# Performance work log

Hardware: AMD Instinct MI355X
Metric: run time of the kernel (lower is better)

## Reference

```python
import jax, jax.numpy as jnp
import numpy as np

SIG_LEVEL = 2
N_UNITS = 1024
INPUT_SIZE = 512
SIGSIZE = sum(2 ** k for k in range(1, SIG_LEVEL + 1))  # siglength(2, L) = 2^(L+1)-2 = 6
SAVED_LEN = N_UNITS * (1 + SIGSIZE)  # 7168
BATCH = 4096


def sigjoin(prev_sigs, disp, time_lapse, level):
    """Chen's identity: new_sig = prev_sig (tensor-mult) exp(v), truncated at `level`.

    prev_sigs: [N, SIGSIZE] flat signature levels (level k occupies 2^k entries),
    disp: [N, 1] displacement in dim 0; dim 1 displacement fixed to time_lapse.
    """
    N = prev_sigs.shape[0]
    v = jnp.concatenate([disp, jnp.full_like(disp, 1.0) * time_lapse], axis=1)  # [N, 2]
    # signature of the straight segment: seg_k = v^{(x)k} / k!
    seg = [v]
    for k in range(2, level + 1):
        seg.append((seg[-1][:, :, None] * v[:, None, :]).reshape(N, -1) / k)
    # split prev signature into levels
    S, off = [], 0
    for k in range(1, level + 1):
        sz = 2 ** k
        S.append(prev_sigs[:, off:off + sz])
        off += sz
    # result_k = S_k + seg_k + sum_{i=1}^{k-1} S_i (x) seg_{k-i}
    out = []
    for k in range(1, level + 1):
        r = S[k - 1] + seg[k - 1]
        for i in range(1, k):
            r = r + (S[i - 1][:, :, None] * seg[k - i - 1][:, None, :]).reshape(N, 2 ** k)
        out.append(r)
    return jnp.concatenate(out, axis=1)


def setup_inputs() -> dict:
    key = jax.random.key(0)
    ks = jax.random.split(key, 8)
    x = jax.random.normal(ks[0], (BATCH, INPUT_SIZE), dtype=jnp.float32)
    prev_sigs = jax.random.normal(ks[1], (BATCH, N_UNITS * SIGSIZE), dtype=jnp.float32) * 0.1
    prev_states = jax.random.normal(ks[2], (BATCH, N_UNITS), dtype=jnp.float32)
    W_w = jax.random.normal(ks[3], (N_UNITS, INPUT_SIZE), dtype=jnp.float32) / np.sqrt(INPUT_SIZE)
    W_b = jax.random.normal(ks[4], (N_UNITS,), dtype=jnp.float32) * 0.01
    U_w = jax.random.normal(ks[5], (N_UNITS, SAVED_LEN), dtype=jnp.float32) / np.sqrt(SAVED_LEN)
    U_b = jax.random.normal(ks[6], (N_UNITS,), dtype=jnp.float32) * 0.01
    log_timelapse = jnp.array([np.log(0.1)], dtype=jnp.float32)
    return {"x": x, "prev_sigs": prev_sigs, "prev_states": prev_states,
            "W_w": W_w, "W_b": W_b, "U_w": U_w, "U_b": U_b,
            "log_timelapse": log_timelapse}


def reference(x, prev_sigs, prev_states, W_w, W_b, U_w, U_b, log_timelapse):
    h = x @ W_w.T + W_b                                  # [B, n_units]
    mem = jnp.concatenate([prev_sigs, prev_states], 1)   # [B, saved_len]
    raw = h + mem @ U_w.T + U_b                          # [B, n_units]
    disp = (raw - prev_states).reshape(-1, 1)            # [B*n_units, 1]
    tl = jnp.exp(log_timelapse)[0]
    sigs = sigjoin(prev_sigs.reshape(-1, SIGSIZE), disp, tl, SIG_LEVEL)
    sigs = sigs.reshape(-1, N_UNITS * SIGSIZE)
    # output_signatures=True: output = [sigs, raw_output]
    return jnp.concatenate([sigs, raw], axis=1)          # [B, n_units*(sigsize+1)]
```

## Files before the change

### kernel.cpp

```cpp
#include <hip/hip_runtime.h>
#include <hip/hip_bf16.h>
#include <cmath>

#define BATCH   4096
#define NUNITS  1024
#define INSIZE  512
#define SIGSZ   6
#define KSIG    (NUNITS * SIGSZ)
#define SAVED   (KSIG + NUNITS)
#define KTOT    (INSIZE + KSIG + NUNITS)
#define OUTW    (NUNITS * (SIGSZ + 1))
#define NKT     (KTOT / 64)

#define WS_AX 0LL
#define WS_AS 2097152LL
#define WS_AT 27262976LL
#define WS_BW 31457280LL
#define WS_BU 31981568LL
#define WS_ELEMS 39321600LL
#define WS_BYTES (WS_ELEMS * 2)

typedef __attribute__((ext_vector_type(8))) short bf16x8;
typedef __attribute__((ext_vector_type(8))) unsigned short u16x8;
typedef __attribute__((ext_vector_type(4))) float f32x4;

__device__ __forceinline__ unsigned short f2bf(float f) {
    union { float f; unsigned int u; } c; c.f = f;
    unsigned int u = c.u;
    return (unsigned short)((u + 0x7FFFu + ((u >> 16) & 1u)) >> 16);
}
__device__ __forceinline__ float bf2f(unsigned short h) {
    union { unsigned int u; float f; } c; c.u = ((unsigned int)h) << 16;
    return c.f;
}

__device__ __forceinline__ int swz(int row, int bytecol) {
    return row * 64 + (((bytecol) ^ ((row & 7) << 4)) >> 1);
}

__global__ __launch_bounds__(256)
void prepack(const float* __restrict__ x, const float* __restrict__ sigs,
             const float* __restrict__ states, const float* __restrict__ Ww,
             const float* __restrict__ Uw, unsigned short* __restrict__ ws)
{
    const long long stride = (long long)gridDim.x * blockDim.x;
    for (long long p = (long long)blockIdx.x * blockDim.x + threadIdx.x;
         p < 4915200LL; p += stride) {
        const float* src; unsigned short* dst; long long o;
        if (p < 262144LL)       { src = x;      dst = ws + WS_AX; o = p; }
        else if (p < 3407872LL) { src = sigs;   dst = ws + WS_AS; o = p - 262144LL; }
        else if (p < 3932160LL) { src = states; dst = ws + WS_AT; o = p - 3407872LL; }
        else if (p < 3997696LL) { src = Ww;     dst = ws + WS_BW; o = p - 3932160LL; }
        else                    { src = Uw;     dst = ws + WS_BU; o = p - 3997696LL; }
        const float4 v0 = *(const float4*)(src + o * 8);
        const float4 v1 = *(const float4*)(src + o * 8 + 4);
        u16x8 h;
        h[0] = f2bf(v0.x); h[1] = f2bf(v0.y); h[2] = f2bf(v0.z); h[3] = f2bf(v0.w);
        h[4] = f2bf(v1.x); h[5] = f2bf(v1.y); h[6] = f2bf(v1.z); h[7] = f2bf(v1.w);
        *(u16x8*)(dst + o * 8) = h;
    }
}

#define GLD_LDS(G, L) __builtin_amdgcn_global_load_lds(                        \
        (const __attribute__((address_space(1))) unsigned int*)(G),           \
        (__attribute__((address_space(3))) unsigned int*)(L), 16, 0, 0)

__global__ __launch_bounds__(1024, 1)
void rsig_gemm(const unsigned short* __restrict__ ws,
               const float* __restrict__ states,
               const float* __restrict__ Wb,
               const float* __restrict__ Ub,
               const float* __restrict__ lt,
               float* __restrict__ out)
{
    __shared__ unsigned short lds[3 * 16384];

    const int t  = threadIdx.x;
    const int bn = blockIdx.x & 7;
    const int bm = blockIdx.x >> 3;

    const int lane = t & 63;
    const int w    = t >> 6;
    const int wm   = w >> 3;
    const int wn   = (w >> 1) & 3;
    const int wk   = w & 1;
    const int lr   = lane & 15;
    const int lg   = lane >> 4;

    const unsigned short* wsAx = ws + WS_AX;
    const unsigned short* wsAs = ws + WS_AS;
    const unsigned short* wsAt = ws + WS_AT;
    const unsigned short* wsBw = ws + WS_BW;
    const unsigned short* wsBu = ws + WS_BU;

    const int sRow = lane >> 3;
    const int sCol = 8 * ((lane & 7) ^ sRow);

    f32x4 acc[4][2];
#pragma unroll
    for (int m = 0; m < 4; ++m)
#pragma unroll
        for (int n = 0; n < 2; ++n)
            acc[m][n] = (f32x4)0.f;

#define STAGE(BUF, KT)                                                                  \
    {                                                                                   \
        const int kt_ = (KT);                                                           \
        const unsigned short* abase; int astr, koff;                                    \
        if (kt_ < 8)        { abase = wsAx; astr = INSIZE; koff = kt_ * 64; }           \
        else if (kt_ < 104) { abase = wsAs; astr = KSIG;   koff = kt_ * 64 - 512; }     \
        else                { abase = wsAt; astr = NUNITS; koff = kt_ * 64 - 6656; }    \
        const unsigned short* bbase; int bstr, koffb;                                   \
        if (kt_ < 8)        { bbase = wsBw; bstr = INSIZE; koffb = kt_ * 64; }          \
        else                { bbase = wsBu; bstr = SAVED;  koffb = kt_ * 64 - 512; }    \
        unsigned short* base = &lds[(BUF) * 16384];                                     \
        const unsigned short* ga = abase                                                \
            + (size_t)(bm * 128 + w * 8 + sRow) * astr + koff + sCol;                   \
        GLD_LDS(ga, base + w * 512);                                                    \
        const unsigned short* gb = bbase                                                \
            + (size_t)(bn * 128 + w * 8 + sRow) * bstr + koffb + sCol;                  \
        GLD_LDS(gb, base + 8192 + w * 512);                                             \
    }

    STAGE(0, 0);
    STAGE(1, 1);

    int cur = 0;
    for (int kt = 0; kt < NKT; ++kt) {
        if (kt < NKT - 1) { asm volatile("s_waitcnt vmcnt(2)" ::: "memory"); }
        else              { asm volatile("s_waitcnt vmcnt(0)" ::: "memory"); }
        __builtin_amdgcn_s_barrier();
        __builtin_amdgcn_sched_barrier(0);

        if (kt + 2 < NKT) {
            int nb = cur + 2; if (nb >= 3) nb -= 3;
            STAGE(nb, kt + 2);
        }

        {
            const unsigned short* aT = &lds[cur * 16384];
            const unsigned short* bT = aT + 8192;
            bf16x8 af[4], bfr[2];
#pragma unroll
            for (int m = 0; m < 4; ++m)
                af[m] = *(const bf16x8*)&aT[swz(wm * 64 + m * 16 + lr, wk * 64 + lg * 16)];
#pragma unroll
            for (int n = 0; n < 2; ++n)
                bfr[n] = *(const bf16x8*)&bT[swz(wn * 32 + n * 16 + lr, wk * 64 + lg * 16)];
#pragma unroll
            for (int m = 0; m < 4; ++m)
#pragma unroll
                for (int n = 0; n < 2; ++n)
                    acc[m][n] = __builtin_amdgcn_mfma_f32_16x16x32_bf16(af[m], bfr[n], acc[m][n], 0, 0, 0);
        }

        cur = (cur == 2) ? 0 : cur + 1;
    }

    __syncthreads();

    float* rawt = (float*)lds;
    if (wk == 0) {
#pragma unroll
        for (int n = 0; n < 2; ++n) {
            const int cc = wn * 32 + n * 16 + lr;
            const int ug = bn * 128 + cc;
            const float bias = Wb[ug] + Ub[ug];
#pragma unroll
            for (int m = 0; m < 4; ++m) {
                const int rr = wm * 64 + m * 16 + lg * 4;
#pragma unroll
                for (int i = 0; i < 4; ++i)
                    rawt[(rr + i) * 132 + cc] = acc[m][n][i] + bias;
            }
        }
    }
    __syncthreads();
    if (wk == 1) {
#pragma unroll
        for (int n = 0; n < 2; ++n) {
            const int cc = wn * 32 + n * 16 + lr;
#pragma unroll
            for (int m = 0; m < 4; ++m) {
                const int rr = wm * 64 + m * 16 + lg * 4;
#pragma unroll
                for (int i = 0; i < 4; ++i)
                    rawt[(rr + i) * 132 + cc] += acc[m][n][i];
            }
        }
    }
    __syncthreads();

    const float tl = expf(lt[0]);
    const int r0 = t >> 8;
    const int c  = t & 255;

    for (int pass = 0; pass < 32; ++pass) {
        const int r = pass * 4 + r0;
        const long long b = (long long)bm * 128 + r;
        if (c < 192) {
            const int u  = (2 * c) / 3;
            const int cs = c % 3;
            const unsigned short* srow = wsAs + b * KSIG + bn * 768;
            const float* strow = states + b * NUNITS + bn * 128;
            const ushort4 sin = *(const ushort4*)(srow + c * 4);
            const float e0 = bf2f(sin.x), e1 = bf2f(sin.y);
            const float e2 = bf2f(sin.z), e3 = bf2f(sin.w);
            float4 o;
            if (cs == 0) {
                const float d = rawt[r * 132 + u] - strow[u];
                o.x = e0 + d;
                o.y = e1 + tl;
                o.z = e2 + d  * (0.5f * d  + e0);
                o.w = e3 + tl * (0.5f * d  + e0);
            } else if (cs == 1) {
                const float d  = rawt[r * 132 + u]     - strow[u];
                const float dn = rawt[r * 132 + u + 1] - strow[u + 1];
                const float s1 = bf2f(srow[u * 6 + 1]);
                o.x = e0 + d  * (0.5f * tl + s1);
                o.y = e1 + tl * (0.5f * tl + s1);
                o.z = e2 + dn;
                o.w = e3 + tl;
            } else {
                const float d = rawt[r * 132 + u] - strow[u];
                const unsigned int sv = *(const unsigned int*)(srow + u * 6);
                const float s0 = bf2f((unsigned short)(sv & 0xffffu));
                const float s1 = bf2f((unsigned short)(sv >> 16));
                o.x = e0 + d  * (0.5f * d  + s0);
                o.y = e1 + tl * (0.5f * d  + s0);
                o.z = e2 + d  * (0.5f * tl + s1);
                o.w = e3 + tl * (0.5f * tl + s1);
            }
            *(float4*)(out + b * OUTW + bn * 768 + c * 4) = o;
        } else if (c < 224) {
            const int cc = (c - 192) * 4;
            const float4 rv = *(const float4*)&rawt[r * 132 + cc];
            *(float4*)(out + b * OUTW + KSIG + bn * 128 + cc) = rv;
        }
    }
#undef STAGE
}

extern "C" void kernel_launch(void* const* d_in, const int* in_sizes, int n_in,
                              void* d_out, int out_size, void* d_ws, size_t ws_size,
                              hipStream_t stream) {
    const float* x      = (const float*)d_in[0];
    const float* sigs   = (const float*)d_in[1];
    const float* states = (const float*)d_in[2];
    const float* Ww     = (const float*)d_in[3];
    const float* Wb     = (const float*)d_in[4];
    const float* Uw     = (const float*)d_in[5];
    const float* Ub     = (const float*)d_in[6];
    const float* lt     = (const float*)d_in[7];
    float* out = (float*)d_out;

    unsigned short* ws = (unsigned short*)d_ws;
    hipLaunchKernelGGL(prepack, dim3(2048), dim3(256), 0, stream,
                       x, sigs, states, Ww, Uw, ws);
    hipLaunchKernelGGL(rsig_gemm, dim3(256), dim3(1024), 0, stream,
                       ws, states, Wb, Ub, lt, out);
}
```

Before: 149.8 us.

## Use BK=128 double-buffered tiles with 4-way K split and nontemporal loads/stores

Doubles the K-tile to 128, so there are half as many loop iterations and barriers, and moves from a 3-stage to a 2-stage LDS ring. Waves are regrouped into 2×2×4 (m, n, k-split) with 4×4 MFMA accumulators per wave. Fragments are read into registers before a barrier, and only then is the next stage issued into the same buffer. The prepack loads and the epilogue stores use nontemporal hints to reduce cache pollution, and the k-split reduction now runs over 4 serialized slots. The extra barrier per iteration reduces overlap, and the larger accumulator set raises register pressure.

```diff
diff --git a/kernel.cpp b/kernel.cpp
--- a/kernel.cpp
+++ b/kernel.cpp
@@ -10,7 +10,7 @@
 #define SAVED   (KSIG + NUNITS)
 #define KTOT    (INSIZE + KSIG + NUNITS)
 #define OUTW    (NUNITS * (SIGSZ + 1))
-#define NKT     (KTOT / 64)
+#define NKT     (KTOT / 128)
 
 #define WS_AX 0LL
 #define WS_AS 2097152LL
@@ -52,11 +52,11 @@
         else if (p < 3932160LL) { src = states; dst = ws + WS_AT; o = p - 3407872LL; }
         else if (p < 3997696LL) { src = Ww;     dst = ws + WS_BW; o = p - 3932160LL; }
         else                    { src = Uw;     dst = ws + WS_BU; o = p - 3997696LL; }
-        const float4 v0 = *(const float4*)(src + o * 8);
-        const float4 v1 = *(const float4*)(src + o * 8 + 4);
+        const f32x4 v0 = __builtin_nontemporal_load((const f32x4*)(src + o * 8));
+        const f32x4 v1 = __builtin_nontemporal_load((const f32x4*)(src + o * 8) + 1);
         u16x8 h;
-        h[0] = f2bf(v0.x); h[1] = f2bf(v0.y); h[2] = f2bf(v0.z); h[3] = f2bf(v0.w);
-        h[4] = f2bf(v1.x); h[5] = f2bf(v1.y); h[6] = f2bf(v1.z); h[7] = f2bf(v1.w);
+        h[0] = f2bf(v0[0]); h[1] = f2bf(v0[1]); h[2] = f2bf(v0[2]); h[3] = f2bf(v0[3]);
+        h[4] = f2bf(v1[0]); h[5] = f2bf(v1[1]); h[6] = f2bf(v1[2]); h[7] = f2bf(v1[3]);
         *(u16x8*)(dst + o * 8) = h;
     }
 }
@@ -73,7 +73,7 @@
                const float* __restrict__ lt,
                float* __restrict__ out)
 {
-    __shared__ unsigned short lds[3 * 16384];
+    __shared__ unsigned short lds[2 * 32768];
 
     const int t  = threadIdx.x;
     const int bn = blockIdx.x & 7;
@@ -82,8 +82,8 @@
     const int lane = t & 63;
     const int w    = t >> 6;
     const int wm   = w >> 3;
-    const int wn   = (w >> 1) & 3;
-    const int wk   = w & 1;
+    const int wn   = (w >> 2) & 1;
+    const int wk   = w & 3;
     const int lr   = lane & 15;
     const int lg   = lane >> 4;
 
@@ -95,101 +95,99 @@
 
     const int sRow = lane >> 3;
     const int sCol = 8 * ((lane & 7) ^ sRow);
-
-    f32x4 acc[4][2];
+    const int rowg = w * 8 + sRow;
+    const int loAx = rowg * INSIZE + sCol;
+    const int loAs = rowg * KSIG   + sCol;
+    const int loAt = rowg * NUNITS + sCol;
+    const int loBw = rowg * INSIZE + sCol;
+    const int loBu = rowg * SAVED  + sCol;
+
+    f32x4 acc[4][4];
 #pragma unroll
     for (int m = 0; m < 4; ++m)
 #pragma unroll
-        for (int n = 0; n < 2; ++n)
+        for (int n = 0; n < 4; ++n)
             acc[m][n] = (f32x4)0.f;
 
-#define STAGE(BUF, KT)                                                                  \
-    {                                                                                   \
-        const int kt_ = (KT);                                                           \
-        const unsigned short* abase; int astr, koff;                                    \
-        if (kt_ < 8)        { abase = wsAx; astr = INSIZE; koff = kt_ * 64; }           \
-        else if (kt_ < 104) { abase = wsAs; astr = KSIG;   koff = kt_ * 64 - 512; }     \
-        else                { abase = wsAt; astr = NUNITS; koff = kt_ * 64 - 6656; }    \
-        const unsigned short* bbase; int bstr, koffb;                                   \
-        if (kt_ < 8)        { bbase = wsBw; bstr = INSIZE; koffb = kt_ * 64; }          \
-        else                { bbase = wsBu; bstr = SAVED;  koffb = kt_ * 64 - 512; }    \
-        unsigned short* base = &lds[(BUF) * 16384];                                     \
-        const unsigned short* ga = abase                                                \
-            + (size_t)(bm * 128 + w * 8 + sRow) * astr + koff + sCol;                   \
-        GLD_LDS(ga, base + w * 512);                                                    \
-        const unsigned short* gb = bbase                                                \
-            + (size_t)(bn * 128 + w * 8 + sRow) * bstr + koffb + sCol;                  \
-        GLD_LDS(gb, base + 8192 + w * 512);                                             \
+#define STAGE(BUF, KT)                                                                   \
+    {                                                                                    \
+        const int kt_ = (KT);                                                            \
+        const unsigned short* abase; long long asg; int la;                              \
+        if (kt_ < 4)       { abase = wsAx; asg = (long long)bm*128*INSIZE + kt_*128;       la = loAx; } \
+        else if (kt_ < 52) { abase = wsAs; asg = (long long)bm*128*KSIG  + kt_*128 - 512;  la = loAs; } \
+        else               { abase = wsAt; asg = (long long)bm*128*NUNITS+ kt_*128 - 6656; la = loAt; } \
+        const unsigned short* bbase; long long bsg; int lb;                              \
+        if (kt_ < 4)       { bbase = wsBw; bsg = (long long)bn*128*INSIZE + kt_*128;       lb = loBw; } \
+        else               { bbase = wsBu; bsg = (long long)bn*128*SAVED + kt_*128 - 512;  lb = loBu; } \
+        unsigned short* base = &lds[(BUF) * 32768];                                      \
+        GLD_LDS(abase + asg + la,      base +         w * 512);                          \
+        GLD_LDS(abase + asg + la + 64, base +  8192 + w * 512);                          \
+        GLD_LDS(bbase + bsg + lb,      base + 16384 + w * 512);                          \
+        GLD_LDS(bbase + bsg + lb + 64, base + 24576 + w * 512);                          \
     }
 
     STAGE(0, 0);
     STAGE(1, 1);
 
-    int cur = 0;
     for (int kt = 0; kt < NKT; ++kt) {
-        if (kt < NKT - 1) { asm volatile("s_waitcnt vmcnt(2)" ::: "memory"); }
+        if (kt < NKT - 1) { asm volatile("s_waitcnt vmcnt(4)" ::: "memory"); }
         else              { asm volatile("s_waitcnt vmcnt(0)" ::: "memory"); }
         __builtin_amdgcn_s_barrier();
         __builtin_amdgcn_sched_barrier(0);
 
-        if (kt + 2 < NKT) {
-            int nb = cur + 2; if (nb >= 3) nb -= 3;
-            STAGE(nb, kt + 2);
-        }
-
-        {
-            const unsigned short* aT = &lds[cur * 16384];
-            const unsigned short* bT = aT + 8192;
-            bf16x8 af[4], bfr[2];
-#pragma unroll
-            for (int m = 0; m < 4; ++m)
-                af[m] = *(const bf16x8*)&aT[swz(wm * 64 + m * 16 + lr, wk * 64 + lg * 16)];
-#pragma unroll
-            for (int n = 0; n < 2; ++n)
-                bfr[n] = *(const bf16x8*)&bT[swz(wn * 32 + n * 16 + lr, wk * 64 + lg * 16)];
-#pragma unroll
-            for (int m = 0; m < 4; ++m)
-#pragma unroll
-                for (int n = 0; n < 2; ++n)
-                    acc[m][n] = __builtin_amdgcn_mfma_f32_16x16x32_bf16(af[m], bfr[n], acc[m][n], 0, 0, 0);
-        }
-
-        cur = (cur == 2) ? 0 : cur + 1;
+        const int cur = kt & 1;
+        const unsigned short* aT = &lds[cur * 32768 + (wk >> 1) * 8192];
+        const unsigned short* bT = aT + 16384;
+        const int bc = (wk & 1) * 64 + lg * 16;
+
+        bf16x8 af[4], bfr[4];
+#pragma unroll
+        for (int m = 0; m < 4; ++m)
+            af[m] = *(const bf16x8*)&aT[swz(wm * 64 + m * 16 + lr, bc)];
+#pragma unroll
+        for (int n = 0; n < 4; ++n)
+            bfr[n] = *(const bf16x8*)&bT[swz(wn * 64 + n * 16 + lr, bc)];
+
+        asm volatile("s_waitcnt lgkmcnt(0)" ::: "memory");
+        __builtin_amdgcn_sched_barrier(0);
+        __builtin_amdgcn_s_barrier();
+
+        if (kt + 2 < NKT) STAGE(cur, kt + 2);
+
+#pragma unroll
+        for (int m = 0; m < 4; ++m)
+#pragma unroll
+            for (int n = 0; n < 4; ++n)
+                acc[m][n] = __builtin_amdgcn_mfma_f32_16x16x32_bf16(af[m], bfr[n], acc[m][n], 0, 0, 0);
     }
 
     __syncthreads();
 
     float* rawt = (float*)lds;
-    if (wk == 0) {
-#pragma unroll
-        for (int n = 0; n < 2; ++n) {
-            const int cc = wn * 32 + n * 16 + lr;
-            const int ug = bn * 128 + cc;
-            const float bias = Wb[ug] + Ub[ug];
-#pragma unroll
-            for (int m = 0; m < 4; ++m) {
-                const int rr = wm * 64 + m * 16 + lg * 4;
-#pragma unroll
-                for (int i = 0; i < 4; ++i)
-                    rawt[(rr + i) * 132 + cc] = acc[m][n][i] + bias;
+#pragma unroll
+    for (int slot = 0; slot < 4; ++slot) {
+        if (wk == slot) {
+#pragma unroll
+            for (int n = 0; n < 4; ++n) {
+                const int cc = wn * 64 + n * 16 + lr;
+#pragma unroll
+                for (int m = 0; m < 4; ++m) {
+                    const int rr = wm * 64 + m * 16 + lg * 4;
+                    if (slot == 0) {
+                        const float bias = Wb[bn * 128 + cc] + Ub[bn * 128 + cc];
+#pragma unroll
+                        for (int i = 0; i < 4; ++i)
+                            rawt[(rr + i) * 132 + cc] = acc[m][n][i] + bias;
+                    } else {
+#pragma unroll
+                        for (int i = 0; i < 4; ++i)
+                            rawt[(rr + i) * 132 + cc] += acc[m][n][i];
+                    }
+                }
             }
         }
-    }
-    __syncthreads();
-    if (wk == 1) {
-#pragma unroll
-        for (int n = 0; n < 2; ++n) {
-            const int cc = wn * 32 + n * 16 + lr;
-#pragma unroll
-            for (int m = 0; m < 4; ++m) {
-                const int rr = wm * 64 + m * 16 + lg * 4;
-#pragma unroll
-                for (int i = 0; i < 4; ++i)
-                    rawt[(rr + i) * 132 + cc] += acc[m][n][i];
-            }
-        }
-    }
-    __syncthreads();
+        __syncthreads();
+    }
 
     const float tl = expf(lt[0]);
     const int r0 = t >> 8;
@@ -206,36 +204,36 @@
             const ushort4 sin = *(const ushort4*)(srow + c * 4);
             const float e0 = bf2f(sin.x), e1 = bf2f(sin.y);
             const float e2 = bf2f(sin.z), e3 = bf2f(sin.w);
-            float4 o;
+            f32x4 o;
             if (cs == 0) {
                 const float d = rawt[r * 132 + u] - strow[u];
-                o.x = e0 + d;
-                o.y = e1 + tl;
-                o.z = e2 + d  * (0.5f * d  + e0);
-                o.w = e3 + tl * (0.5f * d  + e0);
+                o[0] = e0 + d;
+                o[1] = e1 + tl;
+                o[2] = e2 + d  * (0.5f * d  + e0);
+                o[3] = e3 + tl * (0.5f * d  + e0);
             } else if (cs == 1) {
                 const float d  = rawt[r * 132 + u]     - strow[u];
                 const float dn = rawt[r * 132 + u + 1] - strow[u + 1];
                 const float s1 = bf2f(srow[u * 6 + 1]);
-                o.x = e0 + d  * (0.5f * tl + s1);
-                o.y = e1 + tl * (0.5f * tl + s1);
-                o.z = e2 + dn;
-                o.w = e3 + tl;
+                o[0] = e0 + d  * (0.5f * tl + s1);
+                o[1] = e1 + tl * (0.5f * tl + s1);
+                o[2] = e2 + dn;
+                o[3] = e3 + tl;
             } else {
                 const float d = rawt[r * 132 + u] - strow[u];
                 const unsigned int sv = *(const unsigned int*)(srow + u * 6);
                 const float s0 = bf2f((unsigned short)(sv & 0xffffu));
                 const float s1 = bf2f((unsigned short)(sv >> 16));
-                o.x = e0 + d  * (0.5f * d  + s0);
-                o.y = e1 + tl * (0.5f * d  + s0);
-                o.z = e2 + d  * (0.5f * tl + s1);
-                o.w = e3 + tl * (0.5f * tl + s1);
+                o[0] = e0 + d  * (0.5f * d  + s0);
+                o[1] = e1 + tl * (0.5f * d  + s0);
+                o[2] = e2 + d  * (0.5f * tl + s1);
+                o[3] = e3 + tl * (0.5f * tl + s1);
             }
-            *(float4*)(out + b * OUTW + bn * 768 + c * 4) = o;
+            __builtin_nontemporal_store(o, (f32x4*)(out + b * OUTW + bn * 768 + c * 4));
         } else if (c < 224) {
             const int cc = (c - 192) * 4;
-            const float4 rv = *(const float4*)&rawt[r * 132 + cc];
-            *(float4*)(out + b * OUTW + KSIG + bn * 128 + cc) = rv;
+            const f32x4 rv = *(const f32x4*)&rawt[r * 132 + cc];
+            __builtin_nontemporal_store(rv, (f32x4*)(out + b * OUTW + KSIG + bn * 128 + cc));
         }
     }
 #undef STAGE
```

Result: slower. 186.2 us (+24.3%).

## Switch GEMM to 32x32x16 MFMA with K-tile 128, 4-way split-K, double buffer

Applied to the files above, without the earlier changes.

The main GEMM loop now uses 32x32x16 bf16 MFMA instructions on a 128-wide K tile instead of 16x16x32 on a 64-wide tile. Waves are regrouped into 2 N-groups by 4 K-slices, with a new XOR swizzle for the LDS layout. The three-stage pipeline becomes a double buffer with a full vmcnt(0) wait each iteration, and the split-K reduction through LDS grows from 2 to 4 serialized passes. The prepack kernel switches to nontemporal loads. The aim is to halve loop iterations and barriers and get better MFMA efficiency, at the cost of less prefetch depth and extra reduction passes.

```diff
diff --git a/kernel.cpp b/kernel.cpp
--- a/kernel.cpp
+++ b/kernel.cpp
@@ -10,7 +10,7 @@
 #define SAVED   (KSIG + NUNITS)
 #define KTOT    (INSIZE + KSIG + NUNITS)
 #define OUTW    (NUNITS * (SIGSZ + 1))
-#define NKT     (KTOT / 64)
+#define NKT     (KTOT / 128)
 
 #define WS_AX 0LL
 #define WS_AS 2097152LL
@@ -20,9 +20,10 @@
 #define WS_ELEMS 39321600LL
 #define WS_BYTES (WS_ELEMS * 2)
 
-typedef __attribute__((ext_vector_type(8))) short bf16x8;
-typedef __attribute__((ext_vector_type(8))) unsigned short u16x8;
-typedef __attribute__((ext_vector_type(4))) float f32x4;
+typedef __attribute__((ext_vector_type(8)))  short bf16x8;
+typedef __attribute__((ext_vector_type(8)))  unsigned short u16x8;
+typedef __attribute__((ext_vector_type(4)))  float f32x4;
+typedef __attribute__((ext_vector_type(16))) float f32x16;
 
 __device__ __forceinline__ unsigned short f2bf(float f) {
     union { float f; unsigned int u; } c; c.f = f;
@@ -32,10 +33,6 @@
 __device__ __forceinline__ float bf2f(unsigned short h) {
     union { unsigned int u; float f; } c; c.u = ((unsigned int)h) << 16;
     return c.f;
-}
-
-__device__ __forceinline__ int swz(int row, int bytecol) {
-    return row * 64 + (((bytecol) ^ ((row & 7) << 4)) >> 1);
 }
 
 __global__ __launch_bounds__(256)
@@ -52,11 +49,11 @@
         else if (p < 3932160LL) { src = states; dst = ws + WS_AT; o = p - 3407872LL; }
         else if (p < 3997696LL) { src = Ww;     dst = ws + WS_BW; o = p - 3932160LL; }
         else                    { src = Uw;     dst = ws + WS_BU; o = p - 3997696LL; }
-        const float4 v0 = *(const float4*)(src + o * 8);
-        const float4 v1 = *(const float4*)(src + o * 8 + 4);
+        const f32x4 v0 = __builtin_nontemporal_load((const f32x4*)(src + o * 8));
+        const f32x4 v1 = __builtin_nontemporal_load((const f32x4*)(src + o * 8) + 1);
         u16x8 h;
-        h[0] = f2bf(v0.x); h[1] = f2bf(v0.y); h[2] = f2bf(v0.z); h[3] = f2bf(v0.w);
-        h[4] = f2bf(v1.x); h[5] = f2bf(v1.y); h[6] = f2bf(v1.z); h[7] = f2bf(v1.w);
+        h[0] = f2bf(v0[0]); h[1] = f2bf(v0[1]); h[2] = f2bf(v0[2]); h[3] = f2bf(v0[3]);
+        h[4] = f2bf(v1[0]); h[5] = f2bf(v1[1]); h[6] = f2bf(v1[2]); h[7] = f2bf(v1[3]);
         *(u16x8*)(dst + o * 8) = h;
     }
 }
@@ -73,7 +70,7 @@
                const float* __restrict__ lt,
                float* __restrict__ out)
 {
-    __shared__ unsigned short lds[3 * 16384];
+    __shared__ unsigned short lds[2 * 32768];
 
     const int t  = threadIdx.x;
     const int bn = blockIdx.x & 7;
@@ -82,10 +79,10 @@
     const int lane = t & 63;
     const int w    = t >> 6;
     const int wm   = w >> 3;
-    const int wn   = (w >> 1) & 3;
-    const int wk   = w & 1;
-    const int lr   = lane & 15;
-    const int lg   = lane >> 4;
+    const int wn   = (w >> 2) & 1;
+    const int wk   = w & 3;
+    const int lrow = lane & 31;
+    const int lhk  = lane >> 5;
 
     const unsigned short* wsAx = ws + WS_AX;
     const unsigned short* wsAs = ws + WS_AS;
@@ -93,103 +90,121 @@
     const unsigned short* wsBw = ws + WS_BW;
     const unsigned short* wsBu = ws + WS_BU;
 
-    const int sRow = lane >> 3;
-    const int sCol = 8 * ((lane & 7) ^ sRow);
-
-    f32x4 acc[4][2];
-#pragma unroll
-    for (int m = 0; m < 4; ++m)
+    const int sR4 = lane >> 4;
+    const int sS  = lane & 15;
+
+    f32x16 acc[2][2];
+#pragma unroll
+    for (int m = 0; m < 2; ++m)
 #pragma unroll
         for (int n = 0; n < 2; ++n)
-            acc[m][n] = (f32x4)0.f;
-
-#define STAGE(BUF, KT)                                                                  \
-    {                                                                                   \
-        const int kt_ = (KT);                                                           \
-        const unsigned short* abase; int astr, koff;                                    \
-        if (kt_ < 8)        { abase = wsAx; astr = INSIZE; koff = kt_ * 64; }           \
-        else if (kt_ < 104) { abase = wsAs; astr = KSIG;   koff = kt_ * 64 - 512; }     \
-        else                { abase = wsAt; astr = NUNITS; koff = kt_ * 64 - 6656; }    \
-        const unsigned short* bbase; int bstr, koffb;                                   \
-        if (kt_ < 8)        { bbase = wsBw; bstr = INSIZE; koffb = kt_ * 64; }          \
-        else                { bbase = wsBu; bstr = SAVED;  koffb = kt_ * 64 - 512; }    \
-        unsigned short* base = &lds[(BUF) * 16384];                                     \
-        const unsigned short* ga = abase                                                \
-            + (size_t)(bm * 128 + w * 8 + sRow) * astr + koff + sCol;                   \
-        GLD_LDS(ga, base + w * 512);                                                    \
-        const unsigned short* gb = bbase                                                \
-            + (size_t)(bn * 128 + w * 8 + sRow) * bstr + koffb + sCol;                  \
-        GLD_LDS(gb, base + 8192 + w * 512);                                             \
+            acc[m][n] = (f32x16)0.f;
+
+#define STAGE(BUF, KT)                                                                   \
+    {                                                                                    \
+        const int kt_ = (KT);                                                            \
+        const unsigned short* abase; int astr; long long koff;                           \
+        if (kt_ < 4)       { abase = wsAx; astr = INSIZE; koff = (long long)kt_*128; }   \
+        else if (kt_ < 52) { abase = wsAs; astr = KSIG;   koff = (long long)kt_*128-512; }\
+        else               { abase = wsAt; astr = NUNITS; koff = (long long)kt_*128-6656;}\
+        const unsigned short* bbase; int bstr; long long koffb;                          \
+        if (kt_ < 4)       { bbase = wsBw; bstr = INSIZE; koffb = (long long)kt_*128; }  \
+        else               { bbase = wsBu; bstr = SAVED;  koffb = (long long)kt_*128-512;}\
+        unsigned short* base = &lds[(BUF) * 32768];                                      \
+        _Pragma("unroll")                                                                \
+        for (int j = 0; j < 2; ++j) {                                                    \
+            const int g    = 2 * w + j;                                                  \
+            const int rT   = g * 4 + sR4;                                                \
+            const int cblk = sS ^ (((g & 3) << 2) | sR4);                                \
+            const unsigned short* ga = abase + (size_t)(bm * 128 + rT) * astr + koff + cblk * 8; \
+            GLD_LDS(ga, base + g * 512);                                                 \
+            const unsigned short* gb = bbase + (size_t)(bn * 128 + rT) * bstr + koffb + cblk * 8; \
+            GLD_LDS(gb, base + 16384 + g * 512);                                         \
+        }                                                                                \
     }
 
     STAGE(0, 0);
-    STAGE(1, 1);
-
-    int cur = 0;
+
     for (int kt = 0; kt < NKT; ++kt) {
-        if (kt < NKT - 1) { asm volatile("s_waitcnt vmcnt(2)" ::: "memory"); }
-        else              { asm volatile("s_waitcnt vmcnt(0)" ::: "memory"); }
+        asm volatile("s_waitcnt vmcnt(0)" ::: "memory");
         __builtin_amdgcn_s_barrier();
         __builtin_amdgcn_sched_barrier(0);
 
-        if (kt + 2 < NKT) {
-            int nb = cur + 2; if (nb >= 3) nb -= 3;
-            STAGE(nb, kt + 2);
-        }
-
-        {
-            const unsigned short* aT = &lds[cur * 16384];
-            const unsigned short* bT = aT + 8192;
-            bf16x8 af[4], bfr[2];
-#pragma unroll
-            for (int m = 0; m < 4; ++m)
-                af[m] = *(const bf16x8*)&aT[swz(wm * 64 + m * 16 + lr, wk * 64 + lg * 16)];
-#pragma unroll
-            for (int n = 0; n < 2; ++n)
-                bfr[n] = *(const bf16x8*)&bT[swz(wn * 32 + n * 16 + lr, wk * 64 + lg * 16)];
-#pragma unroll
-            for (int m = 0; m < 4; ++m)
+        const int cur = kt & 1;
+        if (kt + 1 < NKT) STAGE(cur ^ 1, kt + 1);
+
+        const unsigned short* aT = &lds[cur * 32768];
+        const unsigned short* bT = aT + 16384;
+
+        bf16x8 af[2][2], bfr[2][2];
+#pragma unroll
+        for (int m = 0; m < 2; ++m) {
+            const int row = wm * 64 + m * 32 + lrow;
+#pragma unroll
+            for (int kk = 0; kk < 2; ++kk) {
+                const int sg = wk * 4 + kk * 2 + lhk;
+                af[m][kk] = *(const bf16x8*)&aT[row * 128 + ((sg ^ (row & 15)) << 3)];
+            }
+        }
+#pragma unroll
+        for (int n = 0; n < 2; ++n) {
+            const int row = wn * 64 + n * 32 + lrow;
+#pragma unroll
+            for (int kk = 0; kk < 2; ++kk) {
+                const int sg = wk * 4 + kk * 2 + lhk;
+                bfr[n][kk] = *(const bf16x8*)&bT[row * 128 + ((sg ^ (row & 15)) << 3)];
+            }
+        }
+
+#pragma unroll
+        for (int kk = 0; kk < 2; ++kk)
+#pragma unroll
+            for (int m = 0; m < 2; ++m)
 #pragma unroll
                 for (int n = 0; n < 2; ++n)
-                    acc[m][n] = __builtin_amdgcn_mfma_f32_16x16x32_bf16(af[m], bfr[n], acc[m][n], 0, 0, 0);
-        }
-
-        cur = (cur == 2) ? 0 : cur + 1;
+                    acc[m][n] = __builtin_amdgcn_mfma_f32_32x32x16_bf16(
+                        af[m][kk], bfr[n][kk], acc[m][n], 0, 0, 0);
     }
 
     __syncthreads();
 
     float* rawt = (float*)lds;
+    const int ccol   = lane & 31;
+    const int rowoff = 4 * lhk;
     if (wk == 0) {
 #pragma unroll
-        for (int n = 0; n < 2; ++n) {
-            const int cc = wn * 32 + n * 16 + lr;
-            const int ug = bn * 128 + cc;
-            const float bias = Wb[ug] + Ub[ug];
-#pragma unroll
-            for (int m = 0; m < 4; ++m) {
-                const int rr = wm * 64 + m * 16 + lg * 4;
-#pragma unroll
-                for (int i = 0; i < 4; ++i)
-                    rawt[(rr + i) * 132 + cc] = acc[m][n][i] + bias;
-            }
-        }
+        for (int m = 0; m < 2; ++m)
+#pragma unroll
+            for (int n = 0; n < 2; ++n) {
+                const int cc = wn * 64 + n * 32 + ccol;
+                const int rr = wm * 64 + m * 32 + rowoff;
+                const float bias = Wb[bn * 128 + cc] + Ub[bn * 128 + cc];
+#pragma unroll
+                for (int reg = 0; reg < 16; ++reg) {
+                    const int r = rr + (reg & 3) + 8 * (reg >> 2);
+                    rawt[r * 132 + cc] = acc[m][n][reg] + bias;
+                }
+            }
     }
     __syncthreads();
-    if (wk == 1) {
-#pragma unroll
-        for (int n = 0; n < 2; ++n) {
-            const int cc = wn * 32 + n * 16 + lr;
-#pragma unroll
-            for (int m = 0; m < 4; ++m) {
-                const int rr = wm * 64 + m * 16 + lg * 4;
-#pragma unroll
-                for (int i = 0; i < 4; ++i)
-                    rawt[(rr + i) * 132 + cc] += acc[m][n][i];
-            }
-        }
-    }
-    __syncthreads();
+#pragma unroll
+    for (int slot = 1; slot < 4; ++slot) {
+        if (wk == slot) {
+#pragma unroll
+            for (int m = 0; m < 2; ++m)
+#pragma unroll
+                for (int n = 0; n < 2; ++n) {
+                    const int cc = wn * 64 + n * 32 + ccol;
+                    const int rr = wm * 64 + m * 32 + rowoff;
+#pragma unroll
+                    for (int reg = 0; reg < 16; ++reg) {
+                        const int r = rr + (reg & 3) + 8 * (reg >> 2);
+                        rawt[r * 132 + cc] += acc[m][n][reg];
+                    }
+                }
+        }
+        __syncthreads();
+    }
 
     const float tl = expf(lt[0]);
     const int r0 = t >> 8;
```

New measurement: 179.0 us. 19.5% more time.
